# Kernel optimization log

Hardware: AMD Instinct MI355X
Metric: run time of the kernel (lower is better)

## Reference

```python
import jax, jax.numpy as jnp
import numpy as np

HEADS = 16
DIM_HEAD = 64
SCALE = DIM_HEAD ** -0.5

def setup_inputs() -> dict:
    key = jax.random.key(0)
    k1, k2, k3 = jax.random.split(key, 3)
    dim = HEADS * DIM_HEAD  # 1024
    x = jax.random.normal(k1, (2, 4096, dim), dtype=jnp.float32)
    w_qkv = jax.random.normal(k2, (dim, 3 * dim), dtype=jnp.float32) * (dim ** -0.5)
    w_out = jax.random.normal(k3, (dim, dim), dtype=jnp.float32) * (dim ** -0.5)
    return {"x": x, "w_qkv": w_qkv, "w_out": w_out}

def reference(x, w_qkv, w_out):
    b, n, dim = x.shape
    qkv = x @ w_qkv  # (b, n, 3*h*d)
    qkv = qkv.reshape(b, n, 3, HEADS, DIM_HEAD)
    q, k, v = (qkv[:, :, 0], qkv[:, :, 1], qkv[:, :, 2])  # (b, n, h, d)
    q = jnp.swapaxes(q, 1, 2) * SCALE  # (b, h, n, d)
    k = jnp.swapaxes(k, 1, 2)
    v = jnp.swapaxes(v, 1, 2)
    sim = jnp.einsum('bhid,bhjd->bhij', q, k)
    mask_value = -jnp.finfo(sim.dtype).max
    causal_mask = jnp.triu(jnp.ones((n, n), dtype=bool), k=1)
    sim = jnp.where(causal_mask, mask_value, sim)
    attn = jax.nn.softmax(sim, axis=-1)
    out = jnp.einsum('bhij,bhjd->bhid', attn, v)
    out = jnp.swapaxes(out, 1, 2).reshape(b, n, HEADS * DIM_HEAD)
    return out @ w_out
```

## Files before the change

kernel.cpp:

```cpp
#include <hip/hip_runtime.h>
#include <stdint.h>
#include <stddef.h>

typedef __attribute__((ext_vector_type(8))) short bf16x8;
typedef __attribute__((ext_vector_type(4))) float f32x4;
typedef __attribute__((ext_vector_type(4))) unsigned short u16x4;
typedef __attribute__((ext_vector_type(4))) unsigned int u32x4;

#define BATCH 2
#define SEQ 4096
#define NHEADS 16
#define DHEAD 64
#define DIM 1024
#define MTOT 8192
#define N1 3072

__device__ __forceinline__ unsigned short f2bf(float f) {
  union { float f; unsigned u; } x; x.f = f;
  unsigned r = x.u + 0x7fffu + ((x.u >> 16) & 1u);
  return (unsigned short)(r >> 16);
}

__device__ __forceinline__ unsigned pk_bf16(float a, float b) {
  unsigned d;
  asm("v_cvt_pk_bf16_f32 %0, %1, %2" : "=v"(d) : "v"(a), "v"(b));
  return d;
}

__device__ __forceinline__ void gload_lds16(const void* g, void* l) {
  __builtin_amdgcn_global_load_lds(
      (const __attribute__((address_space(1))) void*)g,
      (__attribute__((address_space(3))) void*)l, 16, 0, 0);
}

__global__ __launch_bounds__(256) void cvt_f2b(const float* __restrict__ in,
                                               unsigned short* __restrict__ out,
                                               int n4) {
  int i = blockIdx.x * 256 + threadIdx.x;
  if (i < n4) {
    f32x4 v = ((const f32x4*)in)[i];
    u16x4 o;
#pragma unroll
    for (int j = 0; j < 4; j++) o[j] = f2bf(v[j]);
    ((u16x4*)out)[i] = o;
  }
}

__global__ void transpose_cvt(const float* __restrict__ in,
                              unsigned short* __restrict__ out, int R, int C) {
  __shared__ unsigned short t[32][33];
  int tx = threadIdx.x, ty = threadIdx.y;
  int c0 = blockIdx.x * 32, r0 = blockIdx.y * 32;
#pragma unroll
  for (int i = 0; i < 4; i++)
    t[ty + i * 8][tx] = f2bf(in[(size_t)(r0 + ty + i * 8) * C + c0 + tx]);
  __syncthreads();
#pragma unroll
  for (int i = 0; i < 4; i++)
    out[(size_t)(c0 + ty + i * 8) * R + r0 + tx] = t[tx][ty + i * 8];
}

template <int MODE>
__global__ __launch_bounds__(256) void gemm_bt(
    const unsigned short* __restrict__ A,
    const unsigned short* __restrict__ Bt,
    unsigned short* __restrict__ O0,
    unsigned short* __restrict__ O1,
    unsigned short* __restrict__ O2,
    float* __restrict__ Of,
    int N, int K) {
  __shared__ unsigned short Asl[128][32];
  __shared__ unsigned short Bsl[128][32];
  const int tid = threadIdx.x;
  const int lane = tid & 63, wv = tid >> 6;
  const int wr = wv >> 1, wc = wv & 1;
  const int m0 = blockIdx.x * 128, n0 = blockIdx.y * 128;
  const int lrow = lane >> 2, lcol = (lane & 3) * 8;
  const int fr = lane & 15, kc8 = (lane >> 4) * 8;
  f32x4 acc[4][4] = {};
  for (int k0 = 0; k0 < K; k0 += 32) {
#pragma unroll
    for (int c = 0; c < 2; c++) {
      int r = wv * 32 + c * 16 + lrow;
      gload_lds16(&A[(size_t)(m0 + r) * K + k0 + lcol], &Asl[wv * 32 + c * 16][0]);
      gload_lds16(&Bt[(size_t)(n0 + r) * K + k0 + lcol], &Bsl[wv * 32 + c * 16][0]);
    }
    __syncthreads();
    bf16x8 af[4], bfr[4];
#pragma unroll
    for (int i = 0; i < 4; i++)
      af[i] = *(const bf16x8*)&Asl[wr * 64 + i * 16 + fr][kc8];
#pragma unroll
    for (int j = 0; j < 4; j++)
      bfr[j] = *(const bf16x8*)&Bsl[wc * 64 + j * 16 + fr][kc8];
#pragma unroll
    for (int i = 0; i < 4; i++)
#pragma unroll
      for (int j = 0; j < 4; j++)
        acc[i][j] = __builtin_amdgcn_mfma_f32_16x16x32_bf16(af[i], bfr[j], acc[i][j], 0, 0, 0);
    __syncthreads();
  }
  const int rq = (lane >> 4) * 4;
#pragma unroll
  for (int i = 0; i < 4; i++) {
#pragma unroll
    for (int j = 0; j < 4; j++) {
#pragma unroll
      for (int r = 0; r < 4; r++) {
        int row = m0 + wr * 64 + i * 16 + rq + r;
        int col = n0 + wc * 64 + j * 16 + fr;
        float v = acc[i][j][r];
        if (MODE == 0) {
          int w = col >> 10, rem = col & 1023;
          int h = rem >> 6, d = rem & 63;
          int b = row >> 12, n = row & 4095;
          size_t bh = (size_t)b * NHEADS + h;
          if (w == 0)      O0[(bh * SEQ + n) * DHEAD + d] = f2bf(v * 0.125f);
          else if (w == 1) O1[(bh * SEQ + n) * DHEAD + d] = f2bf(v);
          else             O2[(bh * DHEAD + d) * SEQ + n] = f2bf(v);
        } else {
          Of[(size_t)row * N + col] = v;
        }
      }
    }
  }
}

__device__ __forceinline__ void attn_tile3(
    int qt, const unsigned short* __restrict__ Qp,
    const unsigned short* __restrict__ Kp,
    const unsigned short* __restrict__ Vp,
    unsigned short* __restrict__ AOp,
    unsigned short* __restrict__ Kl,
    unsigned short* __restrict__ Vl,
    int lane, int wv) {
  const int fr = lane & 15, g = lane >> 4;
  const int kc8 = g * 8, rq = g * 4;
  const int sw = fr & 7;
  const int q0 = qt * 64;
  const int srl = lane >> 3;
  const int jl = lane & 7;

  bf16x8 qf0 = *(const bf16x8*)&Qp[(size_t)(q0 + wv * 16 + fr) * DHEAD + kc8];
  bf16x8 qf1 = *(const bf16x8*)&Qp[(size_t)(q0 + wv * 16 + fr) * DHEAD + 32 + kc8];

  f32x4 oacc[4] = {};
  float mrow = -1e30f, lrow = 0.f;

#pragma unroll
  for (int c = 0; c < 2; c++) {
    int seg = wv * 2 + c;
    int r = seg * 8 + srl;
    int j = jl ^ (r & 7);
    gload_lds16(&Kp[(size_t)r * DHEAD + j * 8], Kl + seg * 512);
    gload_lds16(&Vp[(size_t)r * SEQ + j * 8], Vl + seg * 512);
  }
  __syncthreads();

  int cur = 0;
  for (int kt = 0; kt <= qt; kt++) {
    const int ktn = (kt < qt) ? kt + 1 : qt;
    unsigned short* Kc = Kl + cur * 4096;
    unsigned short* Vc = Vl + cur * 4096;
    unsigned short* Kn = Kl + (cur ^ 1) * 4096;
    unsigned short* Vn = Vl + (cur ^ 1) * 4096;
#pragma unroll
    for (int c = 0; c < 2; c++) {
      int seg = wv * 2 + c;
      int r = seg * 8 + srl;
      int j = jl ^ (r & 7);
      gload_lds16(&Kp[(size_t)(ktn * 64 + r) * DHEAD + j * 8], Kn + seg * 512);
      gload_lds16(&Vp[(size_t)r * SEQ + ktn * 64 + j * 8], Vn + seg * 512);
    }
    f32x4 sv[4];
    __builtin_amdgcn_s_setprio(1);
#pragma unroll
    for (int cb = 0; cb < 4; cb++) {
      bf16x8 kf0 = *(const bf16x8*)&Kc[(cb * 16 + fr) * 64 + ((g ^ sw) << 3)];
      bf16x8 kf1 = *(const bf16x8*)&Kc[(cb * 16 + fr) * 64 + (((4 + g) ^ sw) << 3)];
      f32x4 z = {};
      z = __builtin_amdgcn_mfma_f32_16x16x32_bf16(kf0, qf0, z, 0, 0, 0);
      sv[cb] = __builtin_amdgcn_mfma_f32_16x16x32_bf16(kf1, qf1, z, 0, 0, 0);
    }
    __builtin_amdgcn_s_setprio(0);
    if (kt == qt) {
#pragma unroll
      for (int cb = 0; cb < 4; cb++)
#pragma unroll
        for (int r = 0; r < 4; r++)
          if (cb * 16 + rq + r > wv * 16 + fr) sv[cb][r] = -1e30f;
    }
    float c0 = fmaxf(fmaxf(sv[0][0], sv[0][1]), fmaxf(sv[0][2], sv[0][3]));
    float c1 = fmaxf(fmaxf(sv[1][0], sv[1][1]), fmaxf(sv[1][2], sv[1][3]));
    float c2 = fmaxf(fmaxf(sv[2][0], sv[2][1]), fmaxf(sv[2][2], sv[2][3]));
    float c3 = fmaxf(fmaxf(sv[3][0], sv[3][1]), fmaxf(sv[3][2], sv[3][3]));
    float pmax = fmaxf(fmaxf(c0, c1), fmaxf(c2, c3));
    pmax = fmaxf(pmax, __shfl_xor(pmax, 16, 64));
    pmax = fmaxf(pmax, __shfl_xor(pmax, 32, 64));
    if (__any(pmax - mrow > 8.f)) {
      float mnew = fmaxf(mrow, pmax);
      float alpha = __expf(mrow - mnew);
      float a0 = __shfl(alpha, rq + 0, 64);
      float a1 = __shfl(alpha, rq + 1, 64);
      float a2 = __shfl(alpha, rq + 2, 64);
      float a3 = __shfl(alpha, rq + 3, 64);
#pragma unroll
      for (int db = 0; db < 4; db++) {
        oacc[db][0] *= a0; oacc[db][1] *= a1;
        oacc[db][2] *= a2; oacc[db][3] *= a3;
      }
      lrow *= alpha;
      mrow = mnew;
    }
    float p[4][4];
#pragma unroll
    for (int cb = 0; cb < 4; cb++)
#pragma unroll
      for (int r = 0; r < 4; r++)
        p[cb][r] = __expf(sv[cb][r] - mrow);
    float t0 = (p[0][0] + p[0][1]) + (p[0][2] + p[0][3]);
    float t1 = (p[1][0] + p[1][1]) + (p[1][2] + p[1][3]);
    float t2 = (p[2][0] + p[2][1]) + (p[2][2] + p[2][3]);
    float t3 = (p[3][0] + p[3][1]) + (p[3][2] + p[3][3]);
    float lsum = (t0 + t1) + (t2 + t3);
    lsum += __shfl_xor(lsum, 16, 64);
    lsum += __shfl_xor(lsum, 32, 64);
    lrow += lsum;
    unsigned A0 = pk_bf16(p[0][0], p[0][1]), A1 = pk_bf16(p[0][2], p[0][3]);
    unsigned B0 = pk_bf16(p[1][0], p[1][1]), B1 = pk_bf16(p[1][2], p[1][3]);
    unsigned C0 = pk_bf16(p[2][0], p[2][1]), C1 = pk_bf16(p[2][2], p[2][3]);
    unsigned D0 = pk_bf16(p[3][0], p[3][1]), D1 = pk_bf16(p[3][2], p[3][3]);
    const bool lo2 = (g < 2);
    unsigned R0 = __shfl_xor((int)(lo2 ? B0 : A0), 32, 64);
    unsigned R1 = __shfl_xor((int)(lo2 ? B1 : A1), 32, 64);
    unsigned R2 = __shfl_xor((int)(lo2 ? D0 : C0), 32, 64);
    unsigned R3 = __shfl_xor((int)(lo2 ? D1 : C1), 32, 64);
    unsigned o00 = (g == 0) ? A0 : (g == 3) ? B0 : R0;
    unsigned o01 = (g == 0) ? A1 : (g == 3) ? B1 : R1;
    unsigned o10 = (g == 0) ? C0 : (g == 3) ? D0 : R2;
    unsigned o11 = (g == 0) ? C1 : (g == 3) ? D1 : R3;
    unsigned p00 = (g == 1) ? A0 : (g == 2) ? B0 : R0;
    unsigned p01 = (g == 1) ? A1 : (g == 2) ? B1 : R1;
    unsigned p10 = (g == 1) ? C0 : (g == 2) ? D0 : R2;
    unsigned p11 = (g == 1) ? C1 : (g == 2) ? D1 : R3;
    unsigned x00 = __shfl_xor((int)p00, 16, 64);
    unsigned x01 = __shfl_xor((int)p01, 16, 64);
    unsigned x10 = __shfl_xor((int)p10, 16, 64);
    unsigned x11 = __shfl_xor((int)p11, 16, 64);
    const bool odd = (g & 1);
    u32x4 f0, f1;
    f0[0] = odd ? x00 : o00; f0[1] = odd ? x01 : o01;
    f0[2] = odd ? o00 : x00; f0[3] = odd ? o01 : x01;
    f1[0] = odd ? x10 : o10; f1[1] = odd ? x11 : o11;
    f1[2] = odd ? o10 : x10; f1[3] = odd ? o11 : x11;
    bf16x8 pa0 = *(bf16x8*)&f0;
    bf16x8 pa1 = *(bf16x8*)&f1;
    __builtin_amdgcn_s_setprio(1);
#pragma unroll
    for (int db = 0; db < 4; db++) {
      bf16x8 vf0 = *(const bf16x8*)&Vc[(db * 16 + fr) * 64 + ((g ^ sw) << 3)];
      bf16x8 vf1 = *(const bf16x8*)&Vc[(db * 16 + fr) * 64 + (((4 + g) ^ sw) << 3)];
      oacc[db] = __builtin_amdgcn_mfma_f32_16x16x32_bf16(pa0, vf0, oacc[db], 0, 0, 0);
      oacc[db] = __builtin_amdgcn_mfma_f32_16x16x32_bf16(pa1, vf1, oacc[db], 0, 0, 0);
    }
    __builtin_amdgcn_s_setprio(0);
    __syncthreads();
    cur ^= 1;
  }

  float i0 = __builtin_amdgcn_rcpf(__shfl(lrow, rq + 0, 64));
  float i1 = __builtin_amdgcn_rcpf(__shfl(lrow, rq + 1, 64));
  float i2 = __builtin_amdgcn_rcpf(__shfl(lrow, rq + 2, 64));
  float i3 = __builtin_amdgcn_rcpf(__shfl(lrow, rq + 3, 64));
#pragma unroll
  for (int db = 0; db < 4; db++) {
    int nb = q0 + wv * 16 + rq;
    int d = db * 16 + fr;
    AOp[(size_t)(nb + 0) * DIM + d] = f2bf(oacc[db][0] * i0);
    AOp[(size_t)(nb + 1) * DIM + d] = f2bf(oacc[db][1] * i1);
    AOp[(size_t)(nb + 2) * DIM + d] = f2bf(oacc[db][2] * i2);
    AOp[(size_t)(nb + 3) * DIM + d] = f2bf(oacc[db][3] * i3);
  }
}

__global__ __launch_bounds__(256, 4) void attn_causal(
    const unsigned short* __restrict__ Q,
    const unsigned short* __restrict__ Kb,
    const unsigned short* __restrict__ Vt,
    unsigned short* __restrict__ AO) {
  const int id = blockIdx.x;
  const int xcd = id & 7, t = id >> 3;
  const int pi = t & 31, bq = t >> 5;
  const int bh = xcd * 4 + bq;
  const int tid = threadIdx.x, lane = tid & 63, wv = tid >> 6;

  const unsigned short* Qp = Q + (size_t)bh * SEQ * DHEAD;
  const unsigned short* Kp = Kb + (size_t)bh * SEQ * DHEAD;
  const unsigned short* Vp = Vt + (size_t)bh * DHEAD * SEQ;
  const int b = bh >> 4, h = bh & 15;
  unsigned short* AOp = AO + (size_t)b * SEQ * DIM + h * DHEAD;

  __shared__ unsigned short Kl[2][4096];
  __shared__ unsigned short Vl[2][4096];

  attn_tile3(pi, Qp, Kp, Vp, AOp, &Kl[0][0], &Vl[0][0], lane, wv);
  attn_tile3(63 - pi, Qp, Kp, Vp, AOp, &Kl[0][0], &Vl[0][0], lane, wv);
}

extern "C" void kernel_launch(void* const* d_in, const int* in_sizes, int n_in,
                              void* d_out, int out_size, void* d_ws, size_t ws_size,
                              hipStream_t stream) {
  const float* x    = (const float*)d_in[0];
  const float* wqkv = (const float*)d_in[1];
  const float* wout = (const float*)d_in[2];
  float* out = (float*)d_out;

  unsigned short* ws = (unsigned short*)d_ws;
  unsigned short* xb = ws;
  unsigned short* ao = ws;
  unsigned short* wqkv_t = ws + (size_t)MTOT * DIM;
  unsigned short* wout_t = wqkv_t + (size_t)N1 * DIM;
  unsigned short* qb = wout_t + (size_t)DIM * DIM;
  unsigned short* kb = qb + (size_t)BATCH * NHEADS * SEQ * DHEAD;
  unsigned short* vt = kb + (size_t)BATCH * NHEADS * SEQ * DHEAD;

  int n4 = (MTOT * DIM) / 4;
  hipLaunchKernelGGL(cvt_f2b, dim3(n4 / 256), dim3(256), 0, stream, x, xb, n4);

  dim3 tb(32, 8);
  hipLaunchKernelGGL(transpose_cvt, dim3(N1 / 32, DIM / 32), tb, 0, stream,
                     wqkv, wqkv_t, DIM, N1);
  hipLaunchKernelGGL(transpose_cvt, dim3(DIM / 32, DIM / 32), tb, 0, stream,
                     wout, wout_t, DIM, DIM);

  hipLaunchKernelGGL((gemm_bt<0>), dim3(MTOT / 128, N1 / 128), dim3(256), 0, stream,
                     xb, wqkv_t, qb, kb, vt, nullptr, N1, DIM);

  hipLaunchKernelGGL(attn_causal, dim3(32 * 32), dim3(256), 0, stream,
                     qb, kb, vt, ao);

  hipLaunchKernelGGL((gemm_bt<1>), dim3(MTOT / 128, DIM / 128), dim3(256), 0, stream,
                     ao, wout_t, nullptr, nullptr, nullptr, out, DIM, DIM);
}
```

Before: 263.1 us.

## Enlarge attention query tile to 128 rows with two sub-tiles per wave

```diff
diff --git a/kernel.cpp b/kernel.cpp
--- a/kernel.cpp
+++ b/kernel.cpp
@@ -14,6 +14,7 @@
 #define DIM 1024
 #define MTOT 8192
 #define N1 3072
+#define NEGINF -3.0e4f
 
 __device__ __forceinline__ unsigned short f2bf(float f) {
   union { float f; unsigned u; } x; x.f = f;
@@ -126,8 +127,8 @@
   }
 }
 
-__device__ __forceinline__ void attn_tile3(
-    int qt, const unsigned short* __restrict__ Qp,
+__device__ __forceinline__ void attn_tile4(
+    int tq, const unsigned short* __restrict__ Qp,
     const unsigned short* __restrict__ Kp,
     const unsigned short* __restrict__ Vp,
     unsigned short* __restrict__ AOp,
@@ -137,15 +138,21 @@
   const int fr = lane & 15, g = lane >> 4;
   const int kc8 = g * 8, rq = g * 4;
   const int sw = fr & 7;
-  const int q0 = qt * 64;
+  const int q0 = tq * 128;
   const int srl = lane >> 3;
   const int jl = lane & 7;
-
-  bf16x8 qf0 = *(const bf16x8*)&Qp[(size_t)(q0 + wv * 16 + fr) * DHEAD + kc8];
-  bf16x8 qf1 = *(const bf16x8*)&Qp[(size_t)(q0 + wv * 16 + fr) * DHEAD + 32 + kc8];
-
-  f32x4 oacc[4] = {};
-  float mrow = -1e30f, lrow = 0.f;
+  const int ktmax = 2 * tq + 1;
+
+  bf16x8 qf[2][2];
+#pragma unroll
+  for (int s = 0; s < 2; s++)
+#pragma unroll
+    for (int c = 0; c < 2; c++)
+      qf[s][c] = *(const bf16x8*)&Qp[(size_t)(q0 + wv * 32 + s * 16 + fr) * DHEAD + c * 32 + kc8];
+
+  f32x4 oacc[2][4] = {};
+  float mrow[2] = {NEGINF, NEGINF};
+  float lrow[2] = {0.f, 0.f};
 
 #pragma unroll
   for (int c = 0; c < 2; c++) {
@@ -158,8 +165,8 @@
   __syncthreads();
 
   int cur = 0;
-  for (int kt = 0; kt <= qt; kt++) {
-    const int ktn = (kt < qt) ? kt + 1 : qt;
+  for (int kt = 0; kt <= ktmax; kt++) {
+    const int ktn = (kt < ktmax) ? kt + 1 : ktmax;
     unsigned short* Kc = Kl + cur * 4096;
     unsigned short* Vc = Vl + cur * 4096;
     unsigned short* Kn = Kl + (cur ^ 1) * 4096;
@@ -172,125 +179,138 @@
       gload_lds16(&Kp[(size_t)(ktn * 64 + r) * DHEAD + j * 8], Kn + seg * 512);
       gload_lds16(&Vp[(size_t)r * SEQ + ktn * 64 + j * 8], Vn + seg * 512);
     }
-    f32x4 sv[4];
+    f32x4 sv[2][4];
     __builtin_amdgcn_s_setprio(1);
 #pragma unroll
     for (int cb = 0; cb < 4; cb++) {
       bf16x8 kf0 = *(const bf16x8*)&Kc[(cb * 16 + fr) * 64 + ((g ^ sw) << 3)];
       bf16x8 kf1 = *(const bf16x8*)&Kc[(cb * 16 + fr) * 64 + (((4 + g) ^ sw) << 3)];
-      f32x4 z = {};
-      z = __builtin_amdgcn_mfma_f32_16x16x32_bf16(kf0, qf0, z, 0, 0, 0);
-      sv[cb] = __builtin_amdgcn_mfma_f32_16x16x32_bf16(kf1, qf1, z, 0, 0, 0);
+      f32x4 z0 = {};
+      z0 = __builtin_amdgcn_mfma_f32_16x16x32_bf16(kf0, qf[0][0], z0, 0, 0, 0);
+      sv[0][cb] = __builtin_amdgcn_mfma_f32_16x16x32_bf16(kf1, qf[0][1], z0, 0, 0, 0);
+      f32x4 z1 = {};
+      z1 = __builtin_amdgcn_mfma_f32_16x16x32_bf16(kf0, qf[1][0], z1, 0, 0, 0);
+      sv[1][cb] = __builtin_amdgcn_mfma_f32_16x16x32_bf16(kf1, qf[1][1], z1, 0, 0, 0);
     }
     __builtin_amdgcn_s_setprio(0);
-    if (kt == qt) {
-#pragma unroll
-      for (int cb = 0; cb < 4; cb++)
-#pragma unroll
-        for (int r = 0; r < 4; r++)
-          if (cb * 16 + rq + r > wv * 16 + fr) sv[cb][r] = -1e30f;
-    }
-    float c0 = fmaxf(fmaxf(sv[0][0], sv[0][1]), fmaxf(sv[0][2], sv[0][3]));
-    float c1 = fmaxf(fmaxf(sv[1][0], sv[1][1]), fmaxf(sv[1][2], sv[1][3]));
-    float c2 = fmaxf(fmaxf(sv[2][0], sv[2][1]), fmaxf(sv[2][2], sv[2][3]));
-    float c3 = fmaxf(fmaxf(sv[3][0], sv[3][1]), fmaxf(sv[3][2], sv[3][3]));
-    float pmax = fmaxf(fmaxf(c0, c1), fmaxf(c2, c3));
-    pmax = fmaxf(pmax, __shfl_xor(pmax, 16, 64));
-    pmax = fmaxf(pmax, __shfl_xor(pmax, 32, 64));
-    if (__any(pmax - mrow > 8.f)) {
-      float mnew = fmaxf(mrow, pmax);
-      float alpha = __expf(mrow - mnew);
+    if (kt >= 2 * tq) {
+      const int delta = (kt - 2 * tq) << 6;
+#pragma unroll
+      for (int s = 0; s < 2; s++)
+#pragma unroll
+        for (int cb = 0; cb < 4; cb++)
+#pragma unroll
+          for (int r = 0; r < 4; r++)
+            if (cb * 16 + rq + r + delta > wv * 32 + s * 16 + fr)
+              sv[s][cb][r] = NEGINF;
+    }
+    bf16x8 pa[2][2];
+#pragma unroll
+    for (int s = 0; s < 2; s++) {
+      float c0 = fmaxf(fmaxf(sv[s][0][0], sv[s][0][1]), fmaxf(sv[s][0][2], sv[s][0][3]));
+      float c1 = fmaxf(fmaxf(sv[s][1][0], sv[s][1][1]), fmaxf(sv[s][1][2], sv[s][1][3]));
+      float c2 = fmaxf(fmaxf(sv[s][2][0], sv[s][2][1]), fmaxf(sv[s][2][2], sv[s][2][3]));
+      float c3 = fmaxf(fmaxf(sv[s][3][0], sv[s][3][1]), fmaxf(sv[s][3][2], sv[s][3][3]));
+      float pmax = fmaxf(fmaxf(c0, c1), fmaxf(c2, c3));
+      pmax = fmaxf(pmax, __shfl_xor(pmax, 16, 64));
+      pmax = fmaxf(pmax, __shfl_xor(pmax, 32, 64));
+      float mnew = fmaxf(mrow[s], pmax);
+      float alpha = __expf(mrow[s] - mnew);
       float a0 = __shfl(alpha, rq + 0, 64);
       float a1 = __shfl(alpha, rq + 1, 64);
       float a2 = __shfl(alpha, rq + 2, 64);
       float a3 = __shfl(alpha, rq + 3, 64);
 #pragma unroll
       for (int db = 0; db < 4; db++) {
-        oacc[db][0] *= a0; oacc[db][1] *= a1;
-        oacc[db][2] *= a2; oacc[db][3] *= a3;
+        oacc[s][db][0] *= a0; oacc[s][db][1] *= a1;
+        oacc[s][db][2] *= a2; oacc[s][db][3] *= a3;
       }
-      lrow *= alpha;
-      mrow = mnew;
-    }
-    float p[4][4];
-#pragma unroll
-    for (int cb = 0; cb < 4; cb++)
-#pragma unroll
-      for (int r = 0; r < 4; r++)
-        p[cb][r] = __expf(sv[cb][r] - mrow);
-    float t0 = (p[0][0] + p[0][1]) + (p[0][2] + p[0][3]);
-    float t1 = (p[1][0] + p[1][1]) + (p[1][2] + p[1][3]);
-    float t2 = (p[2][0] + p[2][1]) + (p[2][2] + p[2][3]);
-    float t3 = (p[3][0] + p[3][1]) + (p[3][2] + p[3][3]);
-    float lsum = (t0 + t1) + (t2 + t3);
-    lsum += __shfl_xor(lsum, 16, 64);
-    lsum += __shfl_xor(lsum, 32, 64);
-    lrow += lsum;
-    unsigned A0 = pk_bf16(p[0][0], p[0][1]), A1 = pk_bf16(p[0][2], p[0][3]);
-    unsigned B0 = pk_bf16(p[1][0], p[1][1]), B1 = pk_bf16(p[1][2], p[1][3]);
-    unsigned C0 = pk_bf16(p[2][0], p[2][1]), C1 = pk_bf16(p[2][2], p[2][3]);
-    unsigned D0 = pk_bf16(p[3][0], p[3][1]), D1 = pk_bf16(p[3][2], p[3][3]);
-    const bool lo2 = (g < 2);
-    unsigned R0 = __shfl_xor((int)(lo2 ? B0 : A0), 32, 64);
-    unsigned R1 = __shfl_xor((int)(lo2 ? B1 : A1), 32, 64);
-    unsigned R2 = __shfl_xor((int)(lo2 ? D0 : C0), 32, 64);
-    unsigned R3 = __shfl_xor((int)(lo2 ? D1 : C1), 32, 64);
-    unsigned o00 = (g == 0) ? A0 : (g == 3) ? B0 : R0;
-    unsigned o01 = (g == 0) ? A1 : (g == 3) ? B1 : R1;
-    unsigned o10 = (g == 0) ? C0 : (g == 3) ? D0 : R2;
-    unsigned o11 = (g == 0) ? C1 : (g == 3) ? D1 : R3;
-    unsigned p00 = (g == 1) ? A0 : (g == 2) ? B0 : R0;
-    unsigned p01 = (g == 1) ? A1 : (g == 2) ? B1 : R1;
-    unsigned p10 = (g == 1) ? C0 : (g == 2) ? D0 : R2;
-    unsigned p11 = (g == 1) ? C1 : (g == 2) ? D1 : R3;
-    unsigned x00 = __shfl_xor((int)p00, 16, 64);
-    unsigned x01 = __shfl_xor((int)p01, 16, 64);
-    unsigned x10 = __shfl_xor((int)p10, 16, 64);
-    unsigned x11 = __shfl_xor((int)p11, 16, 64);
-    const bool odd = (g & 1);
-    u32x4 f0, f1;
-    f0[0] = odd ? x00 : o00; f0[1] = odd ? x01 : o01;
-    f0[2] = odd ? o00 : x00; f0[3] = odd ? o01 : x01;
-    f1[0] = odd ? x10 : o10; f1[1] = odd ? x11 : o11;
-    f1[2] = odd ? o10 : x10; f1[3] = odd ? o11 : x11;
-    bf16x8 pa0 = *(bf16x8*)&f0;
-    bf16x8 pa1 = *(bf16x8*)&f1;
+      lrow[s] *= alpha;
+      mrow[s] = mnew;
+#pragma unroll
+      for (int cb = 0; cb < 4; cb++)
+#pragma unroll
+        for (int r = 0; r < 4; r++)
+          sv[s][cb][r] = __expf(sv[s][cb][r] - mnew);
+      float t0 = (sv[s][0][0] + sv[s][0][1]) + (sv[s][0][2] + sv[s][0][3]);
+      float t1 = (sv[s][1][0] + sv[s][1][1]) + (sv[s][1][2] + sv[s][1][3]);
+      float t2 = (sv[s][2][0] + sv[s][2][1]) + (sv[s][2][2] + sv[s][2][3]);
+      float t3 = (sv[s][3][0] + sv[s][3][1]) + (sv[s][3][2] + sv[s][3][3]);
+      float lsum = (t0 + t1) + (t2 + t3);
+      lsum += __shfl_xor(lsum, 16, 64);
+      lsum += __shfl_xor(lsum, 32, 64);
+      lrow[s] += lsum;
+      unsigned A0 = pk_bf16(sv[s][0][0], sv[s][0][1]), A1 = pk_bf16(sv[s][0][2], sv[s][0][3]);
+      unsigned B0 = pk_bf16(sv[s][1][0], sv[s][1][1]), B1 = pk_bf16(sv[s][1][2], sv[s][1][3]);
+      unsigned C0 = pk_bf16(sv[s][2][0], sv[s][2][1]), C1 = pk_bf16(sv[s][2][2], sv[s][2][3]);
+      unsigned D0 = pk_bf16(sv[s][3][0], sv[s][3][1]), D1 = pk_bf16(sv[s][3][2], sv[s][3][3]);
+      const bool lo2 = (g < 2);
+      unsigned R0 = __shfl_xor((int)(lo2 ? B0 : A0), 32, 64);
+      unsigned R1 = __shfl_xor((int)(lo2 ? B1 : A1), 32, 64);
+      unsigned R2 = __shfl_xor((int)(lo2 ? D0 : C0), 32, 64);
+      unsigned R3 = __shfl_xor((int)(lo2 ? D1 : C1), 32, 64);
+      unsigned o00 = (g == 0) ? A0 : (g == 3) ? B0 : R0;
+      unsigned o01 = (g == 0) ? A1 : (g == 3) ? B1 : R1;
+      unsigned o10 = (g == 0) ? C0 : (g == 3) ? D0 : R2;
+      unsigned o11 = (g == 0) ? C1 : (g == 3) ? D1 : R3;
+      unsigned p00 = (g == 1) ? A0 : (g == 2) ? B0 : R0;
+      unsigned p01 = (g == 1) ? A1 : (g == 2) ? B1 : R1;
+      unsigned p10 = (g == 1) ? C0 : (g == 2) ? D0 : R2;
+      unsigned p11 = (g == 1) ? C1 : (g == 2) ? D1 : R3;
+      unsigned x00 = __shfl_xor((int)p00, 16, 64);
+      unsigned x01 = __shfl_xor((int)p01, 16, 64);
+      unsigned x10 = __shfl_xor((int)p10, 16, 64);
+      unsigned x11 = __shfl_xor((int)p11, 16, 64);
+      const bool odd = (g & 1);
+      u32x4 f0, f1;
+      f0[0] = odd ? x00 : o00; f0[1] = odd ? x01 : o01;
+      f0[2] = odd ? o00 : x00; f0[3] = odd ? o01 : x01;
+      f1[0] = odd ? x10 : o10; f1[1] = odd ? x11 : o11;
+      f1[2] = odd ? o10 : x10; f1[3] = odd ? o11 : x11;
+      pa[s][0] = *(bf16x8*)&f0;
+      pa[s][1] = *(bf16x8*)&f1;
+    }
     __builtin_amdgcn_s_setprio(1);
 #pragma unroll
     for (int db = 0; db < 4; db++) {
       bf16x8 vf0 = *(const bf16x8*)&Vc[(db * 16 + fr) * 64 + ((g ^ sw) << 3)];
       bf16x8 vf1 = *(const bf16x8*)&Vc[(db * 16 + fr) * 64 + (((4 + g) ^ sw) << 3)];
-      oacc[db] = __builtin_amdgcn_mfma_f32_16x16x32_bf16(pa0, vf0, oacc[db], 0, 0, 0);
-      oacc[db] = __builtin_amdgcn_mfma_f32_16x16x32_bf16(pa1, vf1, oacc[db], 0, 0, 0);
+      oacc[0][db] = __builtin_amdgcn_mfma_f32_16x16x32_bf16(pa[0][0], vf0, oacc[0][db], 0, 0, 0);
+      oacc[0][db] = __builtin_amdgcn_mfma_f32_16x16x32_bf16(pa[0][1], vf1, oacc[0][db], 0, 0, 0);
+      oacc[1][db] = __builtin_amdgcn_mfma_f32_16x16x32_bf16(pa[1][0], vf0, oacc[1][db], 0, 0, 0);
+      oacc[1][db] = __builtin_amdgcn_mfma_f32_16x16x32_bf16(pa[1][1], vf1, oacc[1][db], 0, 0, 0);
     }
     __builtin_amdgcn_s_setprio(0);
     __syncthreads();
     cur ^= 1;
   }
 
-  float i0 = __builtin_amdgcn_rcpf(__shfl(lrow, rq + 0, 64));
-  float i1 = __builtin_amdgcn_rcpf(__shfl(lrow, rq + 1, 64));
-  float i2 = __builtin_amdgcn_rcpf(__shfl(lrow, rq + 2, 64));
-  float i3 = __builtin_amdgcn_rcpf(__shfl(lrow, rq + 3, 64));
-#pragma unroll
-  for (int db = 0; db < 4; db++) {
-    int nb = q0 + wv * 16 + rq;
-    int d = db * 16 + fr;
-    AOp[(size_t)(nb + 0) * DIM + d] = f2bf(oacc[db][0] * i0);
-    AOp[(size_t)(nb + 1) * DIM + d] = f2bf(oacc[db][1] * i1);
-    AOp[(size_t)(nb + 2) * DIM + d] = f2bf(oacc[db][2] * i2);
-    AOp[(size_t)(nb + 3) * DIM + d] = f2bf(oacc[db][3] * i3);
-  }
-}
-
-__global__ __launch_bounds__(256, 4) void attn_causal(
+#pragma unroll
+  for (int s = 0; s < 2; s++) {
+    float i0 = __builtin_amdgcn_rcpf(__shfl(lrow[s], rq + 0, 64));
+    float i1 = __builtin_amdgcn_rcpf(__shfl(lrow[s], rq + 1, 64));
+    float i2 = __builtin_amdgcn_rcpf(__shfl(lrow[s], rq + 2, 64));
+    float i3 = __builtin_amdgcn_rcpf(__shfl(lrow[s], rq + 3, 64));
+    int nb = q0 + wv * 32 + s * 16 + rq;
+#pragma unroll
+    for (int db = 0; db < 4; db++) {
+      int d = db * 16 + fr;
+      AOp[(size_t)(nb + 0) * DIM + d] = f2bf(oacc[s][db][0] * i0);
+      AOp[(size_t)(nb + 1) * DIM + d] = f2bf(oacc[s][db][1] * i1);
+      AOp[(size_t)(nb + 2) * DIM + d] = f2bf(oacc[s][db][2] * i2);
+      AOp[(size_t)(nb + 3) * DIM + d] = f2bf(oacc[s][db][3] * i3);
+    }
+  }
+}
+
+__global__ __launch_bounds__(256, 2) void attn_causal(
     const unsigned short* __restrict__ Q,
     const unsigned short* __restrict__ Kb,
     const unsigned short* __restrict__ Vt,
     unsigned short* __restrict__ AO) {
   const int id = blockIdx.x;
   const int xcd = id & 7, t = id >> 3;
-  const int pi = t & 31, bq = t >> 5;
+  const int pi = t & 15, bq = t >> 4;
   const int bh = xcd * 4 + bq;
   const int tid = threadIdx.x, lane = tid & 63, wv = tid >> 6;
 
@@ -303,8 +323,8 @@
   __shared__ unsigned short Kl[2][4096];
   __shared__ unsigned short Vl[2][4096];
 
-  attn_tile3(pi, Qp, Kp, Vp, AOp, &Kl[0][0], &Vl[0][0], lane, wv);
-  attn_tile3(63 - pi, Qp, Kp, Vp, AOp, &Kl[0][0], &Vl[0][0], lane, wv);
+  attn_tile4(pi, Qp, Kp, Vp, AOp, &Kl[0][0], &Vl[0][0], lane, wv);
+  attn_tile4(31 - pi, Qp, Kp, Vp, AOp, &Kl[0][0], &Vl[0][0], lane, wv);
 }
 
 extern "C" void kernel_launch(void* const* d_in, const int* in_sizes, int n_in,
@@ -336,7 +356,7 @@
   hipLaunchKernelGGL((gemm_bt<0>), dim3(MTOT / 128, N1 / 128), dim3(256), 0, stream,
                      xb, wqkv_t, qb, kb, vt, nullptr, N1, DIM);
 
-  hipLaunchKernelGGL(attn_causal, dim3(32 * 32), dim3(256), 0, stream,
+  hipLaunchKernelGGL(attn_causal, dim3(512), dim3(256), 0, stream,
                      qb, kb, vt, ao);
 
   hipLaunchKernelGGL((gemm_bt<1>), dim3(MTOT / 128, DIM / 128), dim3(256), 0, stream,
```

After: 273.9 us. 4.1% more time.
